# Kernel optimization log

Measured on AMD Instinct MI355X. Metric: run time of the kernel, lower is better.

Reference implementation:

```python
import jax, jax.numpy as jnp
import numpy as np

B, S, H = 8, 2048, 1024
W_SCALE = 0.02  # small init keeps the 2048-step recurrence numerically stable


def setup_inputs() -> dict:
    key = jax.random.key(0)
    ks = jax.random.split(key, 6)
    x = jax.random.normal(ks[0], (B, S, H), dtype=jnp.float32)
    h0 = jnp.zeros((B, H), dtype=jnp.float32)
    # torch Linear y = x @ W.T + b; we store pre-transposed [in, out] matrices
    W_in = jax.random.normal(ks[1], (H, 3 * H), dtype=jnp.float32) * W_SCALE
    b_in = jnp.zeros((3 * H,), dtype=jnp.float32)
    W_gate = jax.random.normal(ks[2], (H, 2 * H), dtype=jnp.float32) * W_SCALE
    b_gate = jnp.zeros((2 * H,), dtype=jnp.float32)
    W_rec = jax.random.normal(ks[3], (H, H), dtype=jnp.float32) * W_SCALE
    b_rec = jnp.zeros((H,), dtype=jnp.float32)
    W_out = jax.random.normal(ks[4], (H, H), dtype=jnp.float32) * W_SCALE
    b_out = jnp.zeros((H,), dtype=jnp.float32)
    return {"x": x, "h0": h0, "W_in": W_in, "b_in": b_in,
            "W_gate": W_gate, "b_gate": b_gate, "W_rec": W_rec, "b_rec": b_rec,
            "W_out": W_out, "b_out": b_out}


def reference(x, h0, W_in, b_in, W_gate, b_gate, W_rec, b_rec, W_out, b_out):
    # input projection, chunk into u, v, w and activate (swish)
    feats = x @ W_in + b_in                      # [B,S,3H]
    u, v, w = jnp.split(feats, 3, axis=-1)
    drive = jax.nn.silu(u) * jax.nn.silu(v) + w  # (1-gate) branch, [B,S,H]

    def step(h, d_t):
        g = h @ W_gate + b_gate                  # [B,2H]
        gv, gt = jnp.split(g, 2, axis=-1)
        gate = jax.nn.sigmoid(gv) * jax.nn.silu(gt)  # GLU gate
        new_h = gate * (h @ W_rec + b_rec) + (1.0 - gate) * d_t
        # dropout is identity in eval mode
        return new_h, new_h

    final_h, hs = jax.lax.scan(step, h0, jnp.swapaxes(drive, 0, 1))  # hs: [S,B,H]
    hs = jnp.swapaxes(hs, 0, 1)                  # [B,S,H]
    out = hs @ W_out + b_out                     # per-timestep output_proj, batched
    return out, final_h
```

## Files before the change

kernel.cpp:

```cpp
#include <hip/hip_runtime.h>

typedef short short8 __attribute__((ext_vector_type(8)));
typedef __bf16 bf16x8 __attribute__((ext_vector_type(8)));
typedef float f32x4 __attribute__((ext_vector_type(4)));
typedef float f32x4v __attribute__((ext_vector_type(4)));
typedef unsigned short u16x4 __attribute__((ext_vector_type(4)));
typedef unsigned int uint2v __attribute__((ext_vector_type(2)));
typedef unsigned long long u64;

__device__ __forceinline__ unsigned short f2b(float f) {
  unsigned x = __builtin_bit_cast(unsigned, f);
  x = x + 0x7fffu + ((x >> 16) & 1u);
  return (unsigned short)(x >> 16);
}
__device__ __forceinline__ float b2f(unsigned short u) {
  unsigned x = ((unsigned)u) << 16;
  return __builtin_bit_cast(float, x);
}
__device__ __forceinline__ f32x4 mfma16(short8 a, short8 b, f32x4 c) {
  return __builtin_amdgcn_mfma_f32_16x16x32_bf16(
      __builtin_bit_cast(bf16x8, a), __builtin_bit_cast(bf16x8, b), c, 0, 0, 0);
}
typedef const __attribute__((address_space(1))) void* gas_p;
typedef __attribute__((address_space(3))) void* las_p;
__device__ __forceinline__ void gload_lds16(const void* g, void* l) {
  __builtin_amdgcn_global_load_lds((gas_p)g, (las_p)l, 16, 0, 0);
}

__global__ __launch_bounds__(256) void k_cvt_bf16(const float* __restrict__ in,
                                                  unsigned short* __restrict__ out,
                                                  int n4) {
  int i = blockIdx.x * 256 + threadIdx.x;
  if (i >= n4) return;
  f32x4v v = *(const f32x4v*)(in + (size_t)i * 4);
  u16x4 o;
  o[0] = f2b(v[0]); o[1] = f2b(v[1]); o[2] = f2b(v[2]); o[3] = f2b(v[3]);
  *(u16x4*)(out + (size_t)i * 4) = o;
}

__global__ __launch_bounds__(256) void k_init_hq(const float* __restrict__ h0,
                                                 unsigned int* __restrict__ hq) {
  int idx = blockIdx.x * 256 + threadIdx.x;
  if (idx >= 8192) return;
  int b = idx >> 10, i = idx & 1023;
  hq[(size_t)b * 2048 + i] = (unsigned int)f2b(h0[idx]);
  hq[(size_t)b * 2048 + 1024 + i] = 0u;
}

__global__ __launch_bounds__(256) void k_transpose_bf16(const float* __restrict__ in,
                                                        unsigned short* __restrict__ out,
                                                        int R, int C) {
  __shared__ unsigned short tile[32][33];
  int c0 = blockIdx.x * 32, r0 = blockIdx.y * 32;
  int tx = threadIdx.x & 31, ty = threadIdx.x >> 5;
#pragma unroll
  for (int i = 0; i < 4; i++) {
    int r = ty + i * 8;
    tile[r][tx] = f2b(in[(size_t)(r0 + r) * C + c0 + tx]);
  }
  __syncthreads();
#pragma unroll
  for (int i = 0; i < 4; i++) {
    int rr = ty + i * 8;
    out[(size_t)(c0 + rr) * R + r0 + tx] = tile[tx][rr];
  }
}

__global__ __launch_bounds__(256) void k_gemm_drive(const unsigned short* __restrict__ xb,
                                                    const unsigned short* __restrict__ WinT,
                                                    const float* __restrict__ b_in,
                                                    unsigned short* __restrict__ drive) {
  __shared__ unsigned short At[128 * 32];
  __shared__ unsigned short Bt[3][64 * 32];
  const int tid = threadIdx.x;
  const int w = tid >> 6, l = tid & 63;
  const int wm = w >> 1, wn = w & 1;
  const int lr = l & 15, lk = (l >> 4) * 8;
  const int m0 = blockIdx.x * 128;
  const int j0 = blockIdx.y * 64;
  f32x4 acc[3][4][2];
#pragma unroll
  for (int s = 0; s < 3; s++)
#pragma unroll
    for (int mi = 0; mi < 4; mi++)
#pragma unroll
      for (int ni = 0; ni < 2; ni++)
#pragma unroll
        for (int e = 0; e < 4; e++) acc[s][mi][ni][e] = 0.f;

  const int sr = tid >> 2;
  const int skb = (tid & 3) * 8;
  for (int kt = 0; kt < 32; kt++) {
    const int k0 = kt * 32;
    gload_lds16(xb + (size_t)(m0 + sr) * 1024 + k0 + skb, &At[w * 512]);
    gload_lds16(xb + (size_t)(m0 + 64 + sr) * 1024 + k0 + skb, &At[2048 + w * 512]);
#pragma unroll
    for (int s = 0; s < 3; s++)
      gload_lds16(WinT + (size_t)(s * 1024 + j0 + sr) * 1024 + k0 + skb, &Bt[s][w * 512]);
    __syncthreads();
    short8 Af[4], Bf[3][2];
#pragma unroll
    for (int mi = 0; mi < 4; mi++)
      Af[mi] = *(const short8*)&At[(wm * 64 + mi * 16 + lr) * 32 + lk];
#pragma unroll
    for (int s = 0; s < 3; s++)
#pragma unroll
      for (int ni = 0; ni < 2; ni++)
        Bf[s][ni] = *(const short8*)&Bt[s][(wn * 32 + ni * 16 + lr) * 32 + lk];
#pragma unroll
    for (int s = 0; s < 3; s++)
#pragma unroll
      for (int mi = 0; mi < 4; mi++)
#pragma unroll
        for (int ni = 0; ni < 2; ni++)
          acc[s][mi][ni] = mfma16(Af[mi], Bf[s][ni], acc[s][mi][ni]);
    __syncthreads();
  }
#pragma unroll
  for (int ni = 0; ni < 2; ni++) {
    const int c = j0 + wn * 32 + ni * 16 + lr;
    const float bu = b_in[c], bv = b_in[1024 + c], bw = b_in[2048 + c];
#pragma unroll
    for (int mi = 0; mi < 4; mi++) {
      const int r0 = m0 + wm * 64 + mi * 16 + (l >> 4) * 4;
#pragma unroll
      for (int e = 0; e < 4; e++) {
        float u = acc[0][mi][ni][e] + bu;
        float v = acc[1][mi][ni][e] + bv;
        float wv = acc[2][mi][ni][e] + bw;
        float su = u / (1.f + __expf(-u));
        float sv = v / (1.f + __expf(-v));
        drive[(size_t)(r0 + e) * 1024 + c] = f2b(su * sv + wv);
      }
    }
  }
}

__global__ __launch_bounds__(832, 1) void k_scan(const unsigned short* __restrict__ WgT,
                                                 const unsigned short* __restrict__ WrT,
                                                 const float* __restrict__ b_gate,
                                                 const float* __restrict__ b_rec,
                                                 const unsigned short* __restrict__ drive,
                                                 unsigned int* __restrict__ hq,
                                                 unsigned short* __restrict__ hs,
                                                 float* __restrict__ final_h) {
  const int g = blockIdx.x;
  const int b = g >> 5;
  const int s = g & 31;
  const int tid = threadIdx.x;
  const int w = tid >> 6, l = tid & 63;

  __shared__ unsigned int tile[12][128];
  __shared__ float buf[2][4][3][32];

  const int mat = w >> 2, kq = w & 3;
  const int lr = l & 15, ko = l >> 4;
  const bool av = (lr == 0);
  short8 Breg[2][8];
  if (w < 12) {
    const unsigned short* WT = (mat == 2) ? WrT : WgT;
    const int rowbase = ((mat == 1) ? 1024 : 0) + s * 32;
#pragma unroll
    for (int t2 = 0; t2 < 2; ++t2)
#pragma unroll
      for (int ks = 0; ks < 8; ++ks)
        Breg[t2][ks] = *(const short8*)&WT[(size_t)(rowbase + t2 * 16 + lr) * 1024 +
                                           kq * 256 + ks * 32 + ko * 8];
  }

  const bool isfin = (w == 12) && (l < 32);
  const int fcol = s * 32 + l;
  float bgv = 0.f, bgt = 0.f, brc = 0.f;
  unsigned short dpf = 0;
  if (isfin) {
    bgv = b_gate[fcol]; bgt = b_gate[1024 + fcol]; brc = b_rec[fcol];
    dpf = drive[(size_t)(b * 2048 + 0) * 1024 + fcol];
  }

  for (int t = 0; t < 2048; ++t) {
    const int p = t & 1;

    if (w < 12) {
      const unsigned tg = (unsigned)t;
      const u64* hb = (const u64*)(hq + (size_t)(b * 2 + p) * 1024) + kq * 128 + 2 * l;
      u64 v0 = 0, v1 = 0;
      unsigned pend = 3u;
      do {
        if (pend & 1u)
          v0 = __hip_atomic_load(hb, __ATOMIC_RELAXED, __HIP_MEMORY_SCOPE_AGENT);
        if (pend & 2u)
          v1 = __hip_atomic_load(hb + 1, __ATOMIC_RELAXED, __HIP_MEMORY_SCOPE_AGENT);
        unsigned np = 0;
        if ((((unsigned)v0 >> 16) != tg) | (((unsigned)(v0 >> 32) >> 16) != tg))
          np |= 1u;
        if ((((unsigned)v1 >> 16) != tg) | (((unsigned)(v1 >> 32) >> 16) != tg))
          np |= 2u;
        pend = np;
      } while (pend);
      uint2v pk;
      pk[0] = __builtin_amdgcn_perm((unsigned)(v0 >> 32), (unsigned)v0, 0x05040100u);
      pk[1] = __builtin_amdgcn_perm((unsigned)(v1 >> 32), (unsigned)v1, 0x05040100u);
      *(uint2v*)&tile[w][2 * l] = pk;

      f32x4 a0, a1;
#pragma unroll
      for (int e = 0; e < 4; ++e) { a0[e] = 0.f; a1[e] = 0.f; }
      const char* base = (const char*)&tile[w][0] + ko * 16;
#pragma unroll
      for (int ks = 0; ks < 8; ++ks) {
        short8 Af;
#pragma unroll
        for (int e = 0; e < 8; ++e) Af[e] = 0;
        if (av) Af = *(const short8*)(base + ks * 64);
        a0 = mfma16(Af, Breg[0][ks], a0);
        a1 = mfma16(Af, Breg[1][ks], a1);
      }
      if (l < 16) {
        buf[p][kq][mat][l] = a0[0];
        buf[p][kq][mat][16 + l] = a1[0];
      }
    }
    __syncthreads();

    if (isfin) {
      const float gv = ((buf[p][0][0][l] + buf[p][1][0][l]) +
                        (buf[p][2][0][l] + buf[p][3][0][l])) + bgv;
      const float gt = ((buf[p][0][1][l] + buf[p][1][1][l]) +
                        (buf[p][2][1][l] + buf[p][3][1][l])) + bgt;
      const float rc = ((buf[p][0][2][l] + buf[p][1][2][l]) +
                        (buf[p][2][2][l] + buf[p][3][2][l])) + brc;
      const float sgv = 1.f / (1.f + __expf(-gv));
      const float sgt = 1.f / (1.f + __expf(-gt));
      const float gate = sgv * gt * sgt;
      const float nh = gate * rc + (1.f - gate) * b2f(dpf);
      const unsigned short nhb = f2b(nh);
      __hip_atomic_store(hq + (size_t)(b * 2 + (p ^ 1)) * 1024 + fcol,
                         (((unsigned)(t + 1)) << 16) | (unsigned)nhb,
                         __ATOMIC_RELAXED, __HIP_MEMORY_SCOPE_AGENT);
      hs[(size_t)(b * 2048 + t) * 1024 + fcol] = nhb;
      if (t == 2047) final_h[b * 1024 + fcol] = nh;
      else dpf = drive[(size_t)(b * 2048 + t + 1) * 1024 + fcol];
    }
  }
}

__global__ __launch_bounds__(256) void k_gemm_out(const unsigned short* __restrict__ hs,
                                                  const unsigned short* __restrict__ WoT,
                                                  const float* __restrict__ b_out,
                                                  float* __restrict__ out) {
  __shared__ unsigned short At[128 * 32];
  __shared__ unsigned short Bt[128 * 32];
  const int tid = threadIdx.x;
  const int w = tid >> 6, l = tid & 63;
  const int wm = w >> 1, wn = w & 1;
  const int lr = l & 15, lk = (l >> 4) * 8;
  const int m0 = blockIdx.x * 128;
  const int n0 = blockIdx.y * 128;
  f32x4 acc[4][4];
#pragma unroll
  for (int mi = 0; mi < 4; mi++)
#pragma unroll
    for (int ni = 0; ni < 4; ni++)
#pragma unroll
      for (int e = 0; e < 4; e++) acc[mi][ni][e] = 0.f;

  const int sr = tid >> 2;
  const int skb = (tid & 3) * 8;
  for (int kt = 0; kt < 32; kt++) {
    const int k0 = kt * 32;
    gload_lds16(hs + (size_t)(m0 + sr) * 1024 + k0 + skb, &At[w * 512]);
    gload_lds16(hs + (size_t)(m0 + 64 + sr) * 1024 + k0 + skb, &At[2048 + w * 512]);
    gload_lds16(WoT + (size_t)(n0 + sr) * 1024 + k0 + skb, &Bt[w * 512]);
    gload_lds16(WoT + (size_t)(n0 + 64 + sr) * 1024 + k0 + skb, &Bt[2048 + w * 512]);
    __syncthreads();
    short8 Af[4], Bf[4];
#pragma unroll
    for (int mi = 0; mi < 4; mi++)
      Af[mi] = *(const short8*)&At[(wm * 64 + mi * 16 + lr) * 32 + lk];
#pragma unroll
    for (int ni = 0; ni < 4; ni++)
      Bf[ni] = *(const short8*)&Bt[(wn * 64 + ni * 16 + lr) * 32 + lk];
#pragma unroll
    for (int mi = 0; mi < 4; mi++)
#pragma unroll
      for (int ni = 0; ni < 4; ni++)
        acc[mi][ni] = mfma16(Af[mi], Bf[ni], acc[mi][ni]);
    __syncthreads();
  }
#pragma unroll
  for (int ni = 0; ni < 4; ni++) {
    const int c = n0 + wn * 64 + ni * 16 + lr;
    const float bo = b_out[c];
#pragma unroll
    for (int mi = 0; mi < 4; mi++) {
      const int r0 = m0 + wm * 64 + mi * 16 + (l >> 4) * 4;
#pragma unroll
      for (int e = 0; e < 4; e++)
        out[(size_t)(r0 + e) * 1024 + c] = acc[mi][ni][e] + bo;
    }
  }
}

extern "C" void kernel_launch(void* const* d_in, const int* in_sizes, int n_in,
                              void* d_out, int out_size, void* d_ws, size_t ws_size,
                              hipStream_t stream) {
  const float* x      = (const float*)d_in[0];
  const float* h0     = (const float*)d_in[1];
  const float* W_in   = (const float*)d_in[2];
  const float* b_in   = (const float*)d_in[3];
  const float* W_gate = (const float*)d_in[4];
  const float* b_gate = (const float*)d_in[5];
  const float* W_rec  = (const float*)d_in[6];
  const float* b_rec  = (const float*)d_in[7];
  const float* W_out  = (const float*)d_in[8];
  const float* b_out  = (const float*)d_in[9];
  float* outp = (float*)d_out;

  size_t off = 0;
  auto alloc = [&](size_t bytes) {
    void* p = (char*)d_ws + off;
    off += (bytes + 255) & ~(size_t)255;
    return p;
  };
  unsigned short* xb    = (unsigned short*)alloc((size_t)16777216 * 2);
  unsigned short* WinT  = (unsigned short*)alloc((size_t)3072 * 1024 * 2);
  unsigned short* WgT   = (unsigned short*)alloc((size_t)2048 * 1024 * 2);
  unsigned short* WrT   = (unsigned short*)alloc((size_t)1024 * 1024 * 2);
  unsigned short* WoT   = (unsigned short*)alloc((size_t)1024 * 1024 * 2);
  unsigned short* drive = (unsigned short*)alloc((size_t)16777216 * 2);
  unsigned short* hs    = (unsigned short*)alloc((size_t)16777216 * 2);
  unsigned int*   hq    = (unsigned int*)alloc((size_t)8 * 2 * 1024 * 4);

  k_cvt_bf16<<<16384, 256, 0, stream>>>(x, xb, 4194304);
  k_transpose_bf16<<<dim3(96, 32), 256, 0, stream>>>(W_in, WinT, 1024, 3072);
  k_transpose_bf16<<<dim3(64, 32), 256, 0, stream>>>(W_gate, WgT, 1024, 2048);
  k_transpose_bf16<<<dim3(32, 32), 256, 0, stream>>>(W_rec, WrT, 1024, 1024);
  k_transpose_bf16<<<dim3(32, 32), 256, 0, stream>>>(W_out, WoT, 1024, 1024);
  k_init_hq<<<32, 256, 0, stream>>>(h0, hq);

  k_gemm_drive<<<dim3(128, 16), 256, 0, stream>>>(xb, WinT, b_in, drive);
  k_scan<<<256, 832, 0, stream>>>(WgT, WrT, b_gate, b_rec, drive, hq,
                                  hs, outp + 16777216);
  k_gemm_out<<<dim3(128, 8), 256, 0, stream>>>(hs, WoT, b_out, outp);
}
```

Baseline: 4.409 ms.

## Shrink scan block to four waves each computing all three matrices

The recurrent scan kernel drops from 13 waves per block (12 MFMA waves plus one finalize wave) to 4 waves. Each wave now holds the weight slices of all three matrices for its K-quarter and reuses the single polled h strip across them. The finalize work moves into wave 0. This cuts redundant polling of the global h buffer and makes the per-step block barrier cheaper. In exchange each wave runs three times as many serial MFMAs per step and holds three times as many weight registers.

Result: faster. 4.033 ms (-8.5%).

```diff
diff --git a/kernel.cpp b/kernel.cpp
--- a/kernel.cpp
+++ b/kernel.cpp
@@ -136,7 +136,7 @@
   }
 }
 
-__global__ __launch_bounds__(832, 1) void k_scan(const unsigned short* __restrict__ WgT,
+__global__ __launch_bounds__(256, 1) void k_scan(const unsigned short* __restrict__ WgT,
                                                  const unsigned short* __restrict__ WrT,
                                                  const float* __restrict__ b_gate,
                                                  const float* __restrict__ b_rec,
@@ -150,25 +150,26 @@
   const int tid = threadIdx.x;
   const int w = tid >> 6, l = tid & 63;
 
-  __shared__ unsigned int tile[12][128];
+  __shared__ unsigned int strip[4][128];
   __shared__ float buf[2][4][3][32];
 
-  const int mat = w >> 2, kq = w & 3;
   const int lr = l & 15, ko = l >> 4;
   const bool av = (lr == 0);
-  short8 Breg[2][8];
-  if (w < 12) {
+  short8 Breg[3][2][8];
+#pragma unroll
+  for (int mat = 0; mat < 3; ++mat) {
     const unsigned short* WT = (mat == 2) ? WrT : WgT;
     const int rowbase = ((mat == 1) ? 1024 : 0) + s * 32;
 #pragma unroll
     for (int t2 = 0; t2 < 2; ++t2)
 #pragma unroll
       for (int ks = 0; ks < 8; ++ks)
-        Breg[t2][ks] = *(const short8*)&WT[(size_t)(rowbase + t2 * 16 + lr) * 1024 +
-                                           kq * 256 + ks * 32 + ko * 8];
-  }
-
-  const bool isfin = (w == 12) && (l < 32);
+        Breg[mat][t2][ks] =
+            *(const short8*)&WT[(size_t)(rowbase + t2 * 16 + lr) * 1024 +
+                                w * 256 + ks * 32 + ko * 8];
+  }
+
+  const bool isfin = (w == 0) && (l < 32);
   const int fcol = s * 32 + l;
   float bgv = 0.f, bgt = 0.f, brc = 0.f;
   unsigned short dpf = 0;
@@ -180,9 +181,9 @@
   for (int t = 0; t < 2048; ++t) {
     const int p = t & 1;
 
-    if (w < 12) {
+    {
       const unsigned tg = (unsigned)t;
-      const u64* hb = (const u64*)(hq + (size_t)(b * 2 + p) * 1024) + kq * 128 + 2 * l;
+      const u64* hb = (const u64*)(hq + (size_t)(b * 2 + p) * 1024) + w * 128 + 2 * l;
       u64 v0 = 0, v1 = 0;
       unsigned pend = 3u;
       do {
@@ -200,24 +201,36 @@
       uint2v pk;
       pk[0] = __builtin_amdgcn_perm((unsigned)(v0 >> 32), (unsigned)v0, 0x05040100u);
       pk[1] = __builtin_amdgcn_perm((unsigned)(v1 >> 32), (unsigned)v1, 0x05040100u);
-      *(uint2v*)&tile[w][2 * l] = pk;
-
-      f32x4 a0, a1;
-#pragma unroll
-      for (int e = 0; e < 4; ++e) { a0[e] = 0.f; a1[e] = 0.f; }
-      const char* base = (const char*)&tile[w][0] + ko * 16;
+      *(uint2v*)&strip[w][2 * l] = pk;
+    }
+
+    {
+      f32x4 acc[3][2];
+#pragma unroll
+      for (int mat = 0; mat < 3; ++mat)
+#pragma unroll
+        for (int t2 = 0; t2 < 2; ++t2)
+#pragma unroll
+          for (int e = 0; e < 4; ++e) acc[mat][t2][e] = 0.f;
+      const char* base = (const char*)&strip[w][0] + ko * 16;
 #pragma unroll
       for (int ks = 0; ks < 8; ++ks) {
         short8 Af;
 #pragma unroll
         for (int e = 0; e < 8; ++e) Af[e] = 0;
         if (av) Af = *(const short8*)(base + ks * 64);
-        a0 = mfma16(Af, Breg[0][ks], a0);
-        a1 = mfma16(Af, Breg[1][ks], a1);
+#pragma unroll
+        for (int mat = 0; mat < 3; ++mat) {
+          acc[mat][0] = mfma16(Af, Breg[mat][0][ks], acc[mat][0]);
+          acc[mat][1] = mfma16(Af, Breg[mat][1][ks], acc[mat][1]);
+        }
       }
       if (l < 16) {
-        buf[p][kq][mat][l] = a0[0];
-        buf[p][kq][mat][16 + l] = a1[0];
+#pragma unroll
+        for (int mat = 0; mat < 3; ++mat) {
+          buf[p][w][mat][l] = acc[mat][0][0];
+          buf[p][w][mat][16 + l] = acc[mat][1][0];
+        }
       }
     }
     __syncthreads();
@@ -339,7 +352,7 @@
   k_init_hq<<<32, 256, 0, stream>>>(h0, hq);
 
   k_gemm_drive<<<dim3(128, 16), 256, 0, stream>>>(xb, WinT, b_in, drive);
-  k_scan<<<256, 832, 0, stream>>>(WgT, WrT, b_gate, b_rec, drive, hq,
+  k_scan<<<256, 256, 0, stream>>>(WgT, WrT, b_gate, b_rec, drive, hq,
                                   hs, outp + 16777216);
   k_gemm_out<<<dim3(128, 8), 256, 0, stream>>>(hs, WoT, b_out, outp);
 }
```
